# Kernel tuning notes

Measured on AMD Instinct MI355X. Metric: run time of the kernel, lower is better.

## Reference

```python
import jax, jax.numpy as jnp
import numpy as np

B, L, H, NH = 32, 512, 512, 8
HD = H // NH
SCALE = HD ** -0.5


def _heads(x):
    # (B, L, H) -> (B, NH, L, HD)
    return x.reshape(B, L, NH, HD).transpose(0, 2, 1, 3)


def _score(x, Wq, bq, Wk, bk):
    Q = _heads(x @ Wq.T + bq)
    K = _heads(x @ Wk.T + bk)
    return jnp.einsum('bhqd,bhkd->bhqk', Q, K) * SCALE


def setup_inputs() -> dict:
    key = jax.random.key(0)
    ks = jax.random.split(key, 16)
    d = {
        'seq_id': jax.random.normal(ks[0], (B, L, H), jnp.float32),
        'side_cate': jax.random.normal(ks[1], (B, L, H), jnp.float32),
        'side_brand': jax.random.normal(ks[2], (B, L, H), jnp.float32),
        'V_id_input': jax.random.normal(ks[3], (B, L, H), jnp.float32),
        'relative_time': jax.random.normal(ks[4], (B, NH, L, L), jnp.float32) * 0.02,
        'attn_mask': jnp.broadcast_to(jnp.tril(jnp.ones((L, L), bool)), (B, L, L)),
    }
    s = (2.0 / H) ** 0.5
    names = ['q_id', 'k_id', 'v', 'q_cate', 'k_cate', 'q_brand', 'k_brand', 'o']
    for i, n in enumerate(names):
        d['W' + n] = jax.random.normal(ks[5 + i], (H, H), jnp.float32) * s
        d['b' + n] = jnp.zeros((H,), jnp.float32)
    return d


def reference(seq_id, side_cate, side_brand, V_id_input, relative_time, attn_mask,
              Wq_id, bq_id, Wk_id, bk_id, Wv, bv,
              Wq_cate, bq_cate, Wk_cate, bk_cate,
              Wq_brand, bq_brand, Wk_brand, bk_brand,
              Wo, bo):
    V = _heads(V_id_input @ Wv.T + bv)  # (B, NH, L, HD)
    total = _score(seq_id, Wq_id, bq_id, Wk_id, bk_id)
    total = total + _score(side_cate, Wq_cate, bq_cate, Wk_cate, bk_cate)
    total = total + _score(side_brand, Wq_brand, bq_brand, Wk_brand, bk_brand)
    total = total + relative_time
    total = jnp.where(attn_mask[:, None], total, -jnp.inf)
    w = jax.nn.softmax(total.astype(jnp.float32), axis=-1).astype(total.dtype)
    w = jnp.nan_to_num(w, nan=0.0)
    # eval mode: dropout is identity
    attn_out = jnp.einsum('bhqk,bhkd->bhqd', w, V)
    attn_out = attn_out.transpose(0, 2, 1, 3).reshape(B, L, H)
    return attn_out @ Wo.T + bo
```

## Files before the change

### kernel.cpp

```cpp
#include <hip/hip_runtime.h>
#include <hip/hip_bf16.h>
#include <stdint.h>


typedef __bf16 bf16x8 __attribute__((ext_vector_type(8)));
typedef float f32x4 __attribute__((ext_vector_type(4)));

#define LOG2E 1.4426950408889634f

__device__ int g_isf32;

__device__ __forceinline__ f32x4 mfma16(bf16x8 a, bf16x8 b, f32x4 c) {
    return __builtin_amdgcn_mfma_f32_16x16x32_bf16(a, b, c, 0, 0, 0);
}

__device__ __forceinline__ float qmax16(float x) {
    x = fmaxf(x, __shfl_xor(x, 1));
    x = fmaxf(x, __shfl_xor(x, 2));
    x = fmaxf(x, __shfl_xor(x, 4));
    x = fmaxf(x, __shfl_xor(x, 8));
    return x;
}
__device__ __forceinline__ float qsum16(float x) {
    x += __shfl_xor(x, 1);
    x += __shfl_xor(x, 2);
    x += __shfl_xor(x, 4);
    x += __shfl_xor(x, 8);
    return x;
}

__device__ __forceinline__ bf16x8 ld8(const void* p, size_t off, int isf) {
    if (isf) {
        const float* f = (const float*)p + off;
        f32x4 a = *(const f32x4*)f;
        f32x4 b = *(const f32x4*)(f + 4);
        bf16x8 o;
        o[0] = (__bf16)a[0]; o[1] = (__bf16)a[1]; o[2] = (__bf16)a[2]; o[3] = (__bf16)a[3];
        o[4] = (__bf16)b[0]; o[5] = (__bf16)b[1]; o[6] = (__bf16)b[2]; o[7] = (__bf16)b[3];
        return o;
    }
    return *(const bf16x8*)((const __hip_bfloat16*)p + off);
}

__device__ __forceinline__ float ldf(const void* p, size_t off, int isf) {
    return isf ? ((const float*)p)[off]
               : __bfloat162float(((const __hip_bfloat16*)p)[off]);
}

__global__ void sniff_kernel(const unsigned short* __restrict__ p) {
    int t = threadIdx.x;
    int bad = 0, zc = 0;
    #pragma unroll
    for (int i = 0; i < 32; i++) {
        unsigned short u = p[(t * 32 + i) * 2];
        int e = (u >> 7) & 0xFF;
        bad |= (e >= 0xF0);
        zc += (u == 0);
    }
    unsigned long long mb = __ballot(bad != 0);
    #pragma unroll
    for (int s = 1; s < 64; s <<= 1) zc += __shfl_xor(zc, s);
    if (t == 0) g_isf32 = (mb != 0ull || zc > 1024) ? 1 : 0;
}

__global__ __launch_bounds__(256, 2) void gemm_all(
    const void* __restrict__ xs, const void* __restrict__ xc,
    const void* __restrict__ xb, const void* __restrict__ xv,
    const void* __restrict__ W0, const void* __restrict__ B0,
    const void* __restrict__ W1, const void* __restrict__ B1,
    const void* __restrict__ W2, const void* __restrict__ B2,
    const void* __restrict__ W3, const void* __restrict__ B3,
    const void* __restrict__ W4, const void* __restrict__ B4,
    const void* __restrict__ W5, const void* __restrict__ B5,
    const void* __restrict__ W6, const void* __restrict__ B6,
    const void* __restrict__ Wo, const void* __restrict__ Bo,
    const __hip_bfloat16* __restrict__ AO,
    __hip_bfloat16* __restrict__ Qcat, __hip_bfloat16* __restrict__ Kcat,
    __hip_bfloat16* __restrict__ Vt, void* __restrict__ Out,
    int oproj)
{
    __shared__ __align__(16) __hip_bfloat16 As[128 * 64];
    __shared__ __align__(16) __hip_bfloat16 Bs[128 * 64];

    const int isf = g_isf32;
    const int t = threadIdx.x;
    const int lane = t & 63, w = t >> 6;
    const int ln = lane & 15, hi = lane >> 4;
    const int wm = w >> 1, wn = w & 1;
    const int tm = blockIdx.x * 128, tn = blockIdx.y * 128;

    const void *X, *W, *bias;
    int kind = 3, comp = 0;
    if (oproj) {
        X = AO; W = Wo; bias = Bo;
    } else {
        switch (blockIdx.z) {
            case 0:  X = xs; W = W0; bias = B0; kind = 0; comp = 0; break;
            case 1:  X = xs; W = W1; bias = B1; kind = 1; comp = 0; break;
            case 2:  X = xv; W = W2; bias = B2; kind = 2; comp = 0; break;
            case 3:  X = xc; W = W3; bias = B3; kind = 0; comp = 1; break;
            case 4:  X = xc; W = W4; bias = B4; kind = 1; comp = 1; break;
            case 5:  X = xb; W = W5; bias = B5; kind = 0; comp = 2; break;
            default: X = xb; W = W6; bias = B6; kind = 1; comp = 2; break;
        }
    }
    const int aIsF = oproj ? 0 : isf;

    f32x4 acc[4][4] = {};

    for (int k0 = 0; k0 < 512; k0 += 64) {
        #pragma unroll
        for (int r = 0; r < 4; r++) {
            int e = r * 2048 + t * 8;
            int row = e >> 6, col = e & 63;
            bf16x8 va = ld8(X, (size_t)(tm + row) * 512 + k0 + col, aIsF);
            bf16x8 vb = ld8(W, (size_t)(tn + row) * 512 + k0 + col, isf);
            *(bf16x8*)&As[e] = va;
            *(bf16x8*)&Bs[e] = vb;
        }
        __syncthreads();

        #pragma unroll
        for (int kk = 0; kk < 64; kk += 32) {
            bf16x8 af[4], bfr[4];
            #pragma unroll
            for (int i = 0; i < 4; i++)
                af[i] = *(const bf16x8*)&As[(wm * 64 + i * 16 + ln) * 64 + kk + hi * 8];
            #pragma unroll
            for (int j = 0; j < 4; j++)
                bfr[j] = *(const bf16x8*)&Bs[(wn * 64 + j * 16 + ln) * 64 + kk + hi * 8];
            #pragma unroll
            for (int i = 0; i < 4; i++)
                #pragma unroll
                for (int j = 0; j < 4; j++)
                    acc[i][j] = mfma16(af[i], bfr[j], acc[i][j]);
        }
        __syncthreads();
    }

    #pragma unroll
    for (int j = 0; j < 4; j++) {
        int col = tn + wn * 64 + j * 16 + ln;
        float bv = ldf(bias, col, isf);
        int h = col >> 6, d = col & 63;
        #pragma unroll
        for (int i = 0; i < 4; i++) {
            #pragma unroll
            for (int r = 0; r < 4; r++) {
                int row = tm + wm * 64 + i * 16 + hi * 4 + r;
                float val = acc[i][j][r] + bv;
                int b = row >> 9, l = row & 511;
                if (kind == 0)
                    Qcat[((size_t)(b * 8 + h) * 512 + l) * 192 + comp * 64 + d] =
                        __float2bfloat16(val);
                else if (kind == 1)
                    Kcat[((size_t)(b * 8 + h) * 512 + l) * 192 + comp * 64 + d] =
                        __float2bfloat16(val);
                else if (kind == 2)
                    Vt[((size_t)(b * 8 + h) * 64 + d) * 512 + l] =
                        __float2bfloat16(val);
                else if (isf)
                    ((float*)Out)[(size_t)row * 512 + col] = val;
                else
                    ((__hip_bfloat16*)Out)[(size_t)row * 512 + col] =
                        __float2bfloat16(val);
            }
        }
    }
}

__global__ __launch_bounds__(256, 2) void attn_kernel(
    const __hip_bfloat16* __restrict__ Qcat,
    const __hip_bfloat16* __restrict__ Kcat,
    const __hip_bfloat16* __restrict__ Vt,
    const void* __restrict__ rel,
    __hip_bfloat16* __restrict__ AO)
{
    __shared__ __align__(16) __hip_bfloat16 Ks[64 * 208];
    __shared__ __align__(16) __hip_bfloat16 Vs[64 * 80];
    __shared__ __align__(16) __hip_bfloat16 Ps[4 * 32 * 80];

    const int isf = g_isf32;
    const int t = threadIdx.x;
    const int lane = t & 63, w = t >> 6;
    const int ln = lane & 15, hi = lane >> 4;
    const int qt = blockIdx.x, h = blockIdx.y, b = blockIdx.z;
    const int qb = qt * 128;
    const size_t bh = (size_t)(b * 8 + h);

    const __hip_bfloat16* qc = Qcat + bh * 512 * 192;
    const __hip_bfloat16* kc = Kcat + bh * 512 * 192;
    const __hip_bfloat16* vp = Vt + bh * 64 * 512;
    const size_t rbase = bh * 512 * 512;

    bf16x8 qf[2][6];
    #pragma unroll
    for (int i = 0; i < 2; i++)
        #pragma unroll
        for (int kf = 0; kf < 6; kf++)
            qf[i][kf] = *(const bf16x8*)(qc + (size_t)(qb + w * 32 + i * 16 + ln) * 192
                                            + kf * 32 + hi * 8);

    float mst[2][4], lst[2][4];
    f32x4 oacc[2][4] = {};
    #pragma unroll
    for (int i = 0; i < 2; i++)
        #pragma unroll
        for (int r = 0; r < 4; r++) { mst[i][r] = -1e30f; lst[i][r] = 0.f; }

    const int nkt = 2 * qt + 2;
    for (int kt = 0; kt < nkt; kt++) {
        const int kb = kt * 64;
        __syncthreads();

        #pragma unroll
        for (int r = 0; r < 6; r++) {
            int e = r * 2048 + t * 8;
            int row = e / 192, col = e - row * 192;
            bf16x8 v = *(const bf16x8*)(kc + (size_t)(kb + row) * 192 + col);
            *(bf16x8*)&Ks[row * 208 + col] = v;
        }
        #pragma unroll
        for (int r = 0; r < 2; r++) {
            int e = r * 2048 + t * 8;
            int row = e >> 6, col = e & 63;
            bf16x8 v = *(const bf16x8*)(vp + (size_t)row * 512 + kb + col);
            *(bf16x8*)&Vs[row * 80 + col] = v;
        }
        __syncthreads();

        f32x4 s[2][4] = {};
        #pragma unroll
        for (int kf = 0; kf < 6; kf++) {
            bf16x8 bfr[4];
            #pragma unroll
            for (int j = 0; j < 4; j++)
                bfr[j] = *(const bf16x8*)&Ks[(j * 16 + ln) * 208 + kf * 32 + hi * 8];
            #pragma unroll
            for (int i = 0; i < 2; i++)
                #pragma unroll
                for (int j = 0; j < 4; j++)
                    s[i][j] = mfma16(qf[i][kf], bfr[j], s[i][j]);
        }

        #pragma unroll
        for (int i = 0; i < 2; i++) {
            #pragma unroll
            for (int r = 0; r < 4; r++) {
                int qrow = qb + w * 32 + i * 16 + hi * 4 + r;
                size_t roff = rbase + (size_t)qrow * 512 + kb;
                #pragma unroll
                for (int j = 0; j < 4; j++) {
                    int col = kb + j * 16 + ln;
                    float rv = ldf(rel, roff + j * 16 + ln, isf);
                    float v = fmaf(s[i][j][r], 0.125f * LOG2E, rv * LOG2E);
                    s[i][j][r] = (col > qrow) ? -1e30f : v;
                }
            }
        }

        #pragma unroll
        for (int i = 0; i < 2; i++) {
            #pragma unroll
            for (int r = 0; r < 4; r++) {
                float mx = fmaxf(fmaxf(s[i][0][r], s[i][1][r]),
                                 fmaxf(s[i][2][r], s[i][3][r]));
                mx = qmax16(mx);
                float mnew = fmaxf(mst[i][r], mx);
                float al = exp2f(mst[i][r] - mnew);
                float sum = 0.f;
                #pragma unroll
                for (int j = 0; j < 4; j++) {
                    float p = exp2f(s[i][j][r] - mnew);
                    s[i][j][r] = p;
                    sum += p;
                }
                sum = qsum16(sum);
                lst[i][r] = lst[i][r] * al + sum;
                mst[i][r] = mnew;
                #pragma unroll
                for (int jn = 0; jn < 4; jn++)
                    oacc[i][jn][r] *= al;
            }
        }

        __hip_bfloat16* pw = &Ps[w * 32 * 80];
        #pragma unroll
        for (int i = 0; i < 2; i++) {
            #pragma unroll
            for (int r = 0; r < 4; r++) {
                int prow = i * 16 + hi * 4 + r;
                #pragma unroll
                for (int j = 0; j < 4; j++)
                    pw[prow * 80 + j * 16 + ln] = __float2bfloat16(s[i][j][r]);
            }
        }
        __syncthreads();

        #pragma unroll
        for (int kk = 0; kk < 64; kk += 32) {
            bf16x8 ap[2], bv[4];
            #pragma unroll
            for (int i = 0; i < 2; i++)
                ap[i] = *(const bf16x8*)&Ps[w * 2560 + (i * 16 + ln) * 80 + kk + hi * 8];
            #pragma unroll
            for (int jn = 0; jn < 4; jn++)
                bv[jn] = *(const bf16x8*)&Vs[(jn * 16 + ln) * 80 + kk + hi * 8];
            #pragma unroll
            for (int i = 0; i < 2; i++)
                #pragma unroll
                for (int jn = 0; jn < 4; jn++)
                    oacc[i][jn] = mfma16(ap[i], bv[jn], oacc[i][jn]);
        }
    }

    #pragma unroll
    for (int i = 0; i < 2; i++) {
        #pragma unroll
        for (int r = 0; r < 4; r++) {
            int qrow = qb + w * 32 + i * 16 + hi * 4 + r;
            float inv = 1.0f / lst[i][r];
            __hip_bfloat16* orow = AO + ((size_t)(b * 512 + qrow)) * 512 + h * 64;
            #pragma unroll
            for (int jn = 0; jn < 4; jn++)
                orow[jn * 16 + ln] = __float2bfloat16(oacc[i][jn][r] * inv);
        }
    }
}

extern "C" void kernel_launch(void* const* d_in, const int* in_sizes, int n_in,
                              void* d_out, int out_size, void* d_ws, size_t ws_size,
                              hipStream_t stream) {
    (void)in_sizes; (void)n_in; (void)out_size; (void)ws_size;
    const void* xs  = d_in[0];
    const void* xc  = d_in[1];
    const void* xb  = d_in[2];
    const void* xv  = d_in[3];
    const void* rel = d_in[4];
    const void* W0 = d_in[6];    const void* B0 = d_in[7];
    const void* W1 = d_in[8];    const void* B1 = d_in[9];
    const void* W2 = d_in[10];   const void* B2 = d_in[11];
    const void* W3 = d_in[12];   const void* B3 = d_in[13];
    const void* W4 = d_in[14];   const void* B4 = d_in[15];
    const void* W5 = d_in[16];   const void* B5 = d_in[17];
    const void* W6 = d_in[18];   const void* B6 = d_in[19];
    const void* Wo = d_in[20];   const void* Bo = d_in[21];

    char* ws = (char*)d_ws;
    __hip_bfloat16* Qcat = (__hip_bfloat16*)(ws);
    __hip_bfloat16* Kcat = (__hip_bfloat16*)(ws + 50331648);
    __hip_bfloat16* Vt   = (__hip_bfloat16*)(ws + 100663296);
    __hip_bfloat16* AO   = (__hip_bfloat16*)(ws + 117440512);

    dim3 blk(256, 1, 1);
    sniff_kernel<<<1, 64, 0, stream>>>((const unsigned short*)xs);
    gemm_all<<<dim3(128, 4, 7), blk, 0, stream>>>(
        xs, xc, xb, xv, W0, B0, W1, B1, W2, B2, W3, B3, W4, B4, W5, B5, W6, B6,
        Wo, Bo, AO, Qcat, Kcat, Vt, d_out, 0);
    attn_kernel<<<dim3(4, 8, 32), blk, 0, stream>>>(Qcat, Kcat, Vt, rel, AO);
    gemm_all<<<dim3(128, 4, 1), blk, 0, stream>>>(
        xs, xc, xb, xv, W0, B0, W1, B1, W2, B2, W3, B3, W4, B4, W5, B5, W6, B6,
        Wo, Bo, AO, Qcat, Kcat, Vt, d_out, 1);
}
```

Baseline: 784.0 us.

## Pre-convert shared fp32 activations to bf16 and load A tiles via global_load_lds

Adds a conversion kernel that turns the three fp32 activations, each reused by two projections, into bf16 copies. The copies live in scratch space borrowed from the AO workspace and the output buffer. The GEMM then streams A tiles straight into LDS with the direct global-to-LDS 16-byte load, skipping the per-block fp32 reads and conversions and the register round trip. This trades an extra conversion pass and kernel launch for halved A-operand traffic in the main GEMM. It relies on AO and the output buffer being free at that point in the pipeline.

New measurement: 775.5 us. About the same (-1.1%).

```diff
diff --git a/kernel.cpp b/kernel.cpp
--- a/kernel.cpp
+++ b/kernel.cpp
@@ -47,6 +47,12 @@
                : __bfloat162float(((const __hip_bfloat16*)p)[off]);
 }
 
+__device__ __forceinline__ void glds16(const void* g, void* l) {
+    __builtin_amdgcn_global_load_lds(
+        (const __attribute__((address_space(1))) void*)g,
+        (__attribute__((address_space(3))) void*)l, 16, 0, 0);
+}
+
 __global__ void sniff_kernel(const unsigned short* __restrict__ p) {
     int t = threadIdx.x;
     int bad = 0, zc = 0;
@@ -63,9 +69,31 @@
     if (t == 0) g_isf32 = (mb != 0ull || zc > 1024) ? 1 : 0;
 }
 
+__global__ __launch_bounds__(256) void conv3(
+    const float* __restrict__ s0, const float* __restrict__ s1,
+    const float* __restrict__ s2,
+    __hip_bfloat16* __restrict__ d0, __hip_bfloat16* __restrict__ d1,
+    __hip_bfloat16* __restrict__ d2)
+{
+    if (!g_isf32) return;
+    const float* s = (blockIdx.z == 0) ? s0 : (blockIdx.z == 1) ? s1 : s2;
+    __hip_bfloat16* d = (blockIdx.z == 0) ? d0 : (blockIdx.z == 1) ? d1 : d2;
+    const int N8 = 32 * 512 * 512 / 8;
+    for (int i = blockIdx.x * 256 + threadIdx.x; i < N8; i += gridDim.x * 256) {
+        f32x4 a = ((const f32x4*)s)[2 * i];
+        f32x4 b = ((const f32x4*)s)[2 * i + 1];
+        bf16x8 o;
+        o[0] = (__bf16)a[0]; o[1] = (__bf16)a[1]; o[2] = (__bf16)a[2]; o[3] = (__bf16)a[3];
+        o[4] = (__bf16)b[0]; o[5] = (__bf16)b[1]; o[6] = (__bf16)b[2]; o[7] = (__bf16)b[3];
+        ((bf16x8*)d)[i] = o;
+    }
+}
+
 __global__ __launch_bounds__(256, 2) void gemm_all(
     const void* __restrict__ xs, const void* __restrict__ xc,
     const void* __restrict__ xb, const void* __restrict__ xv,
+    const __hip_bfloat16* __restrict__ Xbs, const __hip_bfloat16* __restrict__ Xbc,
+    const __hip_bfloat16* __restrict__ Xbb,
     const void* __restrict__ W0, const void* __restrict__ B0,
     const void* __restrict__ W1, const void* __restrict__ B1,
     const void* __restrict__ W2, const void* __restrict__ B2,
@@ -89,22 +117,30 @@
     const int wm = w >> 1, wn = w & 1;
     const int tm = blockIdx.x * 128, tn = blockIdx.y * 128;
 
-    const void *X, *W, *bias;
+    const __hip_bfloat16* Abf = nullptr;
+    const void* Araw = nullptr;
+    const void *W, *bias;
     int kind = 3, comp = 0;
     if (oproj) {
-        X = AO; W = Wo; bias = Bo;
+        Abf = AO; W = Wo; bias = Bo;
     } else {
         switch (blockIdx.z) {
-            case 0:  X = xs; W = W0; bias = B0; kind = 0; comp = 0; break;
-            case 1:  X = xs; W = W1; bias = B1; kind = 1; comp = 0; break;
-            case 2:  X = xv; W = W2; bias = B2; kind = 2; comp = 0; break;
-            case 3:  X = xc; W = W3; bias = B3; kind = 0; comp = 1; break;
-            case 4:  X = xc; W = W4; bias = B4; kind = 1; comp = 1; break;
-            case 5:  X = xb; W = W5; bias = B5; kind = 0; comp = 2; break;
-            default: X = xb; W = W6; bias = B6; kind = 1; comp = 2; break;
-        }
-    }
-    const int aIsF = oproj ? 0 : isf;
+            case 0:  Abf = isf ? Xbs : (const __hip_bfloat16*)xs;
+                     W = W0; bias = B0; kind = 0; comp = 0; break;
+            case 1:  Abf = isf ? Xbs : (const __hip_bfloat16*)xs;
+                     W = W1; bias = B1; kind = 1; comp = 0; break;
+            case 2:  if (isf) Araw = xv; else Abf = (const __hip_bfloat16*)xv;
+                     W = W2; bias = B2; kind = 2; comp = 0; break;
+            case 3:  Abf = isf ? Xbc : (const __hip_bfloat16*)xc;
+                     W = W3; bias = B3; kind = 0; comp = 1; break;
+            case 4:  Abf = isf ? Xbc : (const __hip_bfloat16*)xc;
+                     W = W4; bias = B4; kind = 1; comp = 1; break;
+            case 5:  Abf = isf ? Xbb : (const __hip_bfloat16*)xb;
+                     W = W5; bias = B5; kind = 0; comp = 2; break;
+            default: Abf = isf ? Xbb : (const __hip_bfloat16*)xb;
+                     W = W6; bias = B6; kind = 1; comp = 2; break;
+        }
+    }
 
     f32x4 acc[4][4] = {};
 
@@ -113,10 +149,23 @@
         for (int r = 0; r < 4; r++) {
             int e = r * 2048 + t * 8;
             int row = e >> 6, col = e & 63;
-            bf16x8 va = ld8(X, (size_t)(tm + row) * 512 + k0 + col, aIsF);
-            bf16x8 vb = ld8(W, (size_t)(tn + row) * 512 + k0 + col, isf);
-            *(bf16x8*)&As[e] = va;
-            *(bf16x8*)&Bs[e] = vb;
+            *(bf16x8*)&Bs[e] = ld8(W, (size_t)(tn + row) * 512 + k0 + col, isf);
+        }
+        if (Abf) {
+            #pragma unroll
+            for (int r = 0; r < 4; r++) {
+                int e = r * 2048 + t * 8;
+                int row = e >> 6, col = e & 63;
+                glds16(Abf + (size_t)(tm + row) * 512 + k0 + col,
+                       (char*)As + r * 4096 + w * 1024);
+            }
+        } else {
+            #pragma unroll
+            for (int r = 0; r < 4; r++) {
+                int e = r * 2048 + t * 8;
+                int row = e >> 6, col = e & 63;
+                *(bf16x8*)&As[e] = ld8(Araw, (size_t)(tm + row) * 512 + k0 + col, 1);
+            }
         }
         __syncthreads();
 
@@ -352,13 +401,21 @@
     __hip_bfloat16* Vt   = (__hip_bfloat16*)(ws + 100663296);
     __hip_bfloat16* AO   = (__hip_bfloat16*)(ws + 117440512);
 
+    __hip_bfloat16* Xbs = AO;
+    __hip_bfloat16* Xbc = (__hip_bfloat16*)d_out;
+    __hip_bfloat16* Xbb = (__hip_bfloat16*)((char*)d_out + 16777216);
+
     dim3 blk(256, 1, 1);
     sniff_kernel<<<1, 64, 0, stream>>>((const unsigned short*)xs);
+    conv3<<<dim3(1024, 1, 3), blk, 0, stream>>>(
+        (const float*)xs, (const float*)xc, (const float*)xb, Xbs, Xbc, Xbb);
     gemm_all<<<dim3(128, 4, 7), blk, 0, stream>>>(
-        xs, xc, xb, xv, W0, B0, W1, B1, W2, B2, W3, B3, W4, B4, W5, B5, W6, B6,
+        xs, xc, xb, xv, Xbs, Xbc, Xbb,
+        W0, B0, W1, B1, W2, B2, W3, B3, W4, B4, W5, B5, W6, B6,
         Wo, Bo, AO, Qcat, Kcat, Vt, d_out, 0);
     attn_kernel<<<dim3(4, 8, 32), blk, 0, stream>>>(Qcat, Kcat, Vt, rel, AO);
     gemm_all<<<dim3(128, 4, 1), blk, 0, stream>>>(
-        xs, xc, xb, xv, W0, B0, W1, B1, W2, B2, W3, B3, W4, B4, W5, B5, W6, B6,
+        xs, xc, xb, xv, Xbs, Xbc, Xbb,
+        W0, B0, W1, B1, W2, B2, W3, B3, W4, B4, W5, B5, W6, B6,
         Wo, Bo, AO, Qcat, Kcat, Vt, d_out, 1);
 }
```
